# Performance work log

Measured on AMD Instinct MI355X. Metric: run time of the kernel, lower is better.

The kernel has to match this reference:

```python
import jax, jax.numpy as jnp
import numpy as np

N_NODES = 50000
N_EDGES = 800000
IN_FEATS = 256
OUT_FEATS = 32
NUM_HEADS = 8
NUM_ETYPES = 5


def setup_inputs() -> dict:
    key = jax.random.key(0)
    k1, k2, k3, k4, k5, k6 = jax.random.split(key, 6)
    feat = jax.random.normal(k1, (N_NODES, IN_FEATS), dtype=jnp.float32)
    # xavier_normal-ish scale for fc weight [H*D, in]
    fc_w = jax.random.normal(k2, (NUM_HEADS * OUT_FEATS, IN_FEATS), dtype=jnp.float32) * 0.088
    edge_emb = jax.random.normal(k3, (NUM_ETYPES, NUM_HEADS), dtype=jnp.float32)
    e_feat = jax.random.randint(k4, (N_EDGES,), 0, NUM_ETYPES)
    src = jax.random.randint(k5, (N_EDGES,), 0, N_NODES)
    dst = jax.random.randint(k6, (N_EDGES,), 0, N_NODES)
    return {"feat": feat, "fc_w": fc_w, "edge_emb": edge_emb,
            "e_feat": e_feat, "src": src, "dst": dst}


def reference(feat, fc_w, edge_emb, e_feat, src, dst):
    N = feat.shape[0]
    H, D = NUM_HEADS, OUT_FEATS
    # fc: [N, in] @ [in, H*D] -> [N, H, D]
    feat_src = (feat @ fc_w.T).reshape(N, H, D)
    # per-edge, per-head logits from edge-type embedding: [E, H]
    e = edge_emb[e_feat]
    # edge_softmax: softmax over incoming edges of each dst node, per head
    m = jax.ops.segment_max(e, dst, num_segments=N)          # [N, H]
    ex = jnp.exp(e - m[dst])                                  # [E, H]
    denom = jax.ops.segment_sum(ex, dst, num_segments=N)     # [N, H]
    attn = ex / denom[dst]                                    # [E, H]
    # attn_sum: sum of attention weights arriving at each dst (== 1 w/o dropout)
    attn_sum = jax.ops.segment_sum(attn, dst, num_segments=N)  # [N, H]
    # weighted aggregation: sum_e attn_e * feat_src[src_e]
    msg = feat_src[src] * attn[:, :, None]                    # [E, H, D]
    agg = jax.ops.segment_sum(msg, dst, num_segments=N)      # [N, H, D]
    rst = agg / (attn_sum[:, :, None] + 1e-12)
    return rst, attn
```

## Files before the change

kernel.cpp:

```cpp
#include <hip/hip_runtime.h>

typedef unsigned short u16;
typedef unsigned int u32;
typedef __attribute__((ext_vector_type(8))) short bf16x8;
typedef __attribute__((ext_vector_type(4))) float f32x4;
typedef __attribute__((ext_vector_type(2))) float f32x2;

#define NND 50000
#define NE 800000
#define NH 8
#define ND 32
#define NTY 5

__device__ inline u16 f2bf(float x){
  u32 u = __float_as_uint(x);
  return (u16)((u + 0x7FFFu + ((u >> 16) & 1u)) >> 16);
}

__global__ __launch_bounds__(512, 4) void gemm_k(const float* __restrict__ A,
                                                 const float* __restrict__ W,
                                                 u16* __restrict__ C, int M){
  __shared__ float As[128 * 64];
  __shared__ u16  Ws[256 * 64];
  const int tid  = threadIdx.x;
  const int m0   = blockIdx.x * 128;
  const int lane = tid & 63, wid = tid >> 6;
  const int wm = (wid >> 2) * 64, wn = (wid & 3) * 64;
  const int ml = lane & 15, quad = lane >> 4;

  f32x4 acc[4][4] = {};

  const int ra = tid >> 2, ca = (tid & 3) * 4;
  int rag = m0 + ra; if (rag >= M) rag = M - 1;
  const float* aRow = A + (size_t)rag * 256;
  const int rw = tid >> 1, hw = tid & 1;
  const float* wRow = W + (size_t)rw * 256;

  for (int k0 = 0; k0 < 256; k0 += 64){
    #pragma unroll
    for (int q = 0; q < 4; q++){
      float4 v = *(const float4*)(aRow + k0 + (ca + q) * 4);
      *(float4*)(As + ra * 64 + (((ca + q) ^ (ra & 15)) * 4)) = v;
    }
    #pragma unroll
    for (int q = 0; q < 4; q++){
      int ck = hw * 4 + q;
      float4 u0 = *(const float4*)(wRow + k0 + ck * 8);
      float4 u1 = *(const float4*)(wRow + k0 + ck * 8 + 4);
      ushort4 h0 = make_ushort4(f2bf(u0.x), f2bf(u0.y), f2bf(u0.z), f2bf(u0.w));
      ushort4 h1 = make_ushort4(f2bf(u1.x), f2bf(u1.y), f2bf(u1.z), f2bf(u1.w));
      int cp = ck ^ (rw & 7);
      *(ushort4*)(Ws + rw * 64 + cp * 8) = h0;
      *(ushort4*)(Ws + rw * 64 + cp * 8 + 4) = h1;
    }
    __syncthreads();
    #pragma unroll
    for (int kk = 0; kk < 64; kk += 32){
      bf16x8 af[4], wf[4];
      #pragma unroll
      for (int t = 0; t < 4; t++){
        int r = wm + t * 16 + ml;
        int c0 = (kk >> 2) + quad * 2;
        float4 x0 = *(const float4*)(As + r * 64 + (((c0    ) ^ (r & 15)) * 4));
        float4 x1 = *(const float4*)(As + r * 64 + (((c0 + 1) ^ (r & 15)) * 4));
        af[t] = (bf16x8){ (short)f2bf(x0.x), (short)f2bf(x0.y), (short)f2bf(x0.z), (short)f2bf(x0.w),
                          (short)f2bf(x1.x), (short)f2bf(x1.y), (short)f2bf(x1.z), (short)f2bf(x1.w) };
      }
      #pragma unroll
      for (int t = 0; t < 4; t++){
        int n = wn + t * 16 + ml;
        int c = (kk >> 3) + quad;
        wf[t] = *(const bf16x8*)(Ws + n * 64 + ((c ^ (n & 7)) * 8));
      }
      #pragma unroll
      for (int i = 0; i < 4; i++)
        #pragma unroll
        for (int j = 0; j < 4; j++)
          acc[i][j] = __builtin_amdgcn_mfma_f32_16x16x32_bf16(af[i], wf[j], acc[i][j], 0, 0, 0);
    }
    __syncthreads();
  }
  const size_t qoff = (size_t)(wn >> 6) * NND * 64;
  #pragma unroll
  for (int i = 0; i < 4; i++){
    #pragma unroll
    for (int rr = 0; rr < 4; rr++){
      int row = m0 + wm + i * 16 + quad * 4 + rr;
      if (row < M){
        u16* crow = C + qoff + (size_t)row * 64;
        #pragma unroll
        for (int j = 0; j < 4; j++)
          crow[j * 16 + ml] = f2bf(acc[i][j][rr]);
      }
    }
  }
}

__global__ __launch_bounds__(256) void count_k(const int* __restrict__ dst,
                                               int* __restrict__ deg,
                                               int* __restrict__ epos){
  int e = blockIdx.x * 256 + threadIdx.x;
  if (e < NE) epos[e] = atomicAdd(&deg[dst[e]], 1);
}

__global__ __launch_bounds__(256) void scan1_k(const int* __restrict__ deg,
                                               int* __restrict__ offs,
                                               int* __restrict__ bsum){
  __shared__ int lds[256];
  int b = blockIdx.x, tid = threadIdx.x;
  int base = b * 1024 + tid * 4;
  int d[4]; int tsum = 0;
  #pragma unroll
  for (int j = 0; j < 4; j++){
    int node = base + j;
    int v = (node < NND) ? deg[node] : 0;
    d[j] = tsum; tsum += v;
  }
  lds[tid] = tsum; __syncthreads();
  for (int off = 1; off < 256; off <<= 1){
    int v = (tid >= off) ? lds[tid - off] : 0;
    __syncthreads();
    lds[tid] += v;
    __syncthreads();
  }
  int excl = lds[tid] - tsum;
  #pragma unroll
  for (int j = 0; j < 4; j++)
    if (base + j < NND) offs[base + j] = excl + d[j];
  if (tid == 255) bsum[b] = lds[tid];
}

__global__ __launch_bounds__(64) void scan2_k(const int* __restrict__ bsum,
                                              int* __restrict__ bbase, int nb){
  __shared__ int l[64];
  int tid = threadIdx.x;
  int v = (tid < nb) ? bsum[tid] : 0;
  l[tid] = v; __syncthreads();
  for (int off = 1; off < 64; off <<= 1){
    int u = (tid >= off) ? l[tid - off] : 0;
    __syncthreads();
    l[tid] += u;
    __syncthreads();
  }
  bbase[tid] = l[tid] - v;
}

__global__ __launch_bounds__(256) void scatter_k(const int* __restrict__ dst,
                                                 const int* __restrict__ src,
                                                 const int* __restrict__ ef,
                                                 const int* __restrict__ epos,
                                                 const int* __restrict__ offs,
                                                 const int* __restrict__ bbase,
                                                 int* __restrict__ csr){
  int e = blockIdx.x * 256 + threadIdx.x;
  if (e >= NE) return;
  int d = dst[e];
  int pos = offs[d] + bbase[d >> 10] + epos[e];
  csr[pos] = (src[e] << 7) | ef[e];
}

__global__ __launch_bounds__(256) void attn_k(const int* __restrict__ dst,
                                              const int* __restrict__ ef,
                                              const float* __restrict__ rd,
                                              const float* __restrict__ emb,
                                              float* __restrict__ attn){
  __shared__ float wl[40];
  int tid = threadIdx.x;
  if (tid < 40){
    int t = tid >> 3, h = tid & 7;
    float m = emb[h];
    for (int tt = 1; tt < NTY; ++tt) m = fmaxf(m, emb[tt * 8 + h]);
    wl[tid] = expf(emb[t * 8 + h] - m);
  }
  __syncthreads();
  int e = blockIdx.x * 256 + tid;
  if (e >= NE) return;
  int d = dst[e], t = ef[e];
  float4 r0 = *(const float4*)(rd + (size_t)d * 8);
  float4 r1 = *(const float4*)(rd + (size_t)d * 8 + 4);
  const float* wr = wl + t * 8;
  *(float4*)(attn + (size_t)e * 8)     = make_float4(wr[0]*r0.x, wr[1]*r0.y, wr[2]*r0.z, wr[3]*r0.w);
  *(float4*)(attn + (size_t)e * 8 + 4) = make_float4(wr[4]*r1.x, wr[5]*r1.y, wr[6]*r1.z, wr[7]*r1.w);
}

__device__ inline void acc8(uint4 v, float wt, f32x2* a){
  f32x2 w2; w2.x = wt; w2.y = wt;
  f32x2 t0; t0.x = __uint_as_float(v.x << 16); t0.y = __uint_as_float(v.x & 0xFFFF0000u);
  f32x2 t1; t1.x = __uint_as_float(v.y << 16); t1.y = __uint_as_float(v.y & 0xFFFF0000u);
  f32x2 t2; t2.x = __uint_as_float(v.z << 16); t2.y = __uint_as_float(v.z & 0xFFFF0000u);
  f32x2 t3; t3.x = __uint_as_float(v.w << 16); t3.y = __uint_as_float(v.w & 0xFFFF0000u);
  a[0] += w2 * t0; a[1] += w2 * t1; a[2] += w2 * t2; a[3] += w2 * t3;
}

#define NBLK ((NND + 31) / 32)

__global__ __launch_bounds__(256) void agg_k(const u16* __restrict__ fsrc,
                                             const int* __restrict__ csr,
                                             const int* __restrict__ offs,
                                             const int* __restrict__ bbase,
                                             const int* __restrict__ deg,
                                             const float* __restrict__ emb,
                                             float* __restrict__ rst,
                                             float* __restrict__ rd){
  __shared__ float wl[40];
  int tid = threadIdx.x;
  if (tid < 40){
    int t = tid >> 3, h = tid & 7;
    float m = emb[h];
    for (int tt = 1; tt < NTY; ++tt) m = fmaxf(m, emb[tt * 8 + h]);
    wl[tid] = expf(emb[t * 8 + h] - m);
  }
  __syncthreads();
  const int q  = blockIdx.x / NBLK;
  const int nb = blockIdx.x % NBLK;
  int node = nb * 32 + (tid >> 3);
  if (node >= NND) return;
  const int sl = tid & 7;
  const int h  = 2 * q + (sl >> 2);
  const u16* qbase = fsrc + (size_t)q * (NND * 64) + sl * 8;
  int s = offs[node] + bbase[node >> 10];
  int e = s + deg[node];
  f32x2 a[4]; a[0] = 0.f; a[1] = 0.f; a[2] = 0.f; a[3] = 0.f;
  float ss = 0.f;
  int i = s;
  for (; i + 3 < e; i += 4){
    int p0 = csr[i], p1 = csr[i+1], p2 = csr[i+2], p3 = csr[i+3];
    uint4 v0 = *(const uint4*)(qbase + ((size_t)(p0 >> 7) << 6));
    uint4 v1 = *(const uint4*)(qbase + ((size_t)(p1 >> 7) << 6));
    uint4 v2 = *(const uint4*)(qbase + ((size_t)(p2 >> 7) << 6));
    uint4 v3 = *(const uint4*)(qbase + ((size_t)(p3 >> 7) << 6));
    float w0 = wl[(p0 & 7) * 8 + h];
    float w1 = wl[(p1 & 7) * 8 + h];
    float w2 = wl[(p2 & 7) * 8 + h];
    float w3 = wl[(p3 & 7) * 8 + h];
    acc8(v0, w0, a); acc8(v1, w1, a); acc8(v2, w2, a); acc8(v3, w3, a);
    ss += (w0 + w1) + (w2 + w3);
  }
  for (; i < e; i++){
    int p0 = csr[i];
    uint4 v0 = *(const uint4*)(qbase + ((size_t)(p0 >> 7) << 6));
    float w0 = wl[(p0 & 7) * 8 + h];
    acc8(v0, w0, a);
    ss += w0;
  }
  float inv = 1.0f / (ss + 1e-12f);
  float* orow = rst + (size_t)node * 256 + q * 64 + sl * 8;
  *(float4*)(orow)     = make_float4(a[0].x*inv, a[0].y*inv, a[1].x*inv, a[1].y*inv);
  *(float4*)(orow + 4) = make_float4(a[2].x*inv, a[2].y*inv, a[3].x*inv, a[3].y*inv);
  if ((sl & 3) == 0) rd[(size_t)node * 8 + h] = inv;
}

extern "C" void kernel_launch(void* const* d_in, const int* in_sizes, int n_in,
                              void* d_out, int out_size, void* d_ws, size_t ws_size,
                              hipStream_t stream) {
  const float* feat = (const float*)d_in[0];
  const float* fcw  = (const float*)d_in[1];
  const float* emb  = (const float*)d_in[2];
  const int*   ef   = (const int*)d_in[3];
  const int*   src  = (const int*)d_in[4];
  const int*   dst  = (const int*)d_in[5];

  float* rst  = (float*)d_out;
  float* attn = (float*)d_out + (size_t)NND * NH * ND;

  char* ws = (char*)d_ws;
  size_t o = 0;
  u16* fsrc    = (u16*)(ws + o);   o += (size_t)NND * 256 * 2;
  int* csr     = (int*)(ws + o);   o += (size_t)NE * 4;
  int* epos    = (int*)(ws + o);   o += (size_t)NE * 4;
  int* offs    = (int*)(ws + o);   o += 200064;
  int* deg     = (int*)(ws + o);   o += 200064;
  float* rd    = (float*)(ws + o); o += (size_t)NND * NH * 4;
  int* bsum    = (int*)(ws + o);   o += 256;
  int* bbase   = (int*)(ws + o);   o += 256;

  hipMemsetAsync(deg, 0, (size_t)NND * 4, stream);

  gemm_k<<<391, 512, 0, stream>>>(feat, fcw, fsrc, NND);
  count_k<<<(NE + 255) / 256, 256, 0, stream>>>(dst, deg, epos);
  scan1_k<<<(NND + 1023) / 1024, 256, 0, stream>>>(deg, offs, bsum);
  scan2_k<<<1, 64, 0, stream>>>(bsum, bbase, (NND + 1023) / 1024);
  scatter_k<<<(NE + 255) / 256, 256, 0, stream>>>(dst, src, ef, epos, offs, bbase, csr);
  agg_k<<<4 * NBLK, 256, 0, stream>>>(fsrc, csr, offs, bbase, deg, emb, rst, rd);
  attn_k<<<(NE + 255) / 256, 256, 0, stream>>>(dst, ef, rd, emb, attn);
}
```

Baseline: 276.7 us.

## Pre-convert weights to bf16, stage A as bf16 in LDS, add nontemporal I/O

```diff
diff --git a/kernel.cpp b/kernel.cpp
--- a/kernel.cpp
+++ b/kernel.cpp
@@ -17,11 +17,19 @@
   return (u16)((u + 0x7FFFu + ((u >> 16) & 1u)) >> 16);
 }
 
+__global__ __launch_bounds__(256) void wcvt_k(const float* __restrict__ W,
+                                              u16* __restrict__ Wb){
+  int i = (blockIdx.x * 256 + threadIdx.x) * 4;
+  f32x4 v = __builtin_nontemporal_load((const f32x4*)(W + i));
+  ushort4 h = make_ushort4(f2bf(v[0]), f2bf(v[1]), f2bf(v[2]), f2bf(v[3]));
+  *(ushort4*)(Wb + i) = h;
+}
+
 __global__ __launch_bounds__(512, 4) void gemm_k(const float* __restrict__ A,
-                                                 const float* __restrict__ W,
+                                                 const u16* __restrict__ Wb,
                                                  u16* __restrict__ C, int M){
-  __shared__ float As[128 * 64];
-  __shared__ u16  Ws[256 * 64];
+  __shared__ u16 As[128 * 64];
+  __shared__ u16 Ws[256 * 64];
   const int tid  = threadIdx.x;
   const int m0   = blockIdx.x * 128;
   const int lane = tid & 63, wid = tid >> 6;
@@ -30,47 +38,44 @@
 
   f32x4 acc[4][4] = {};
 
-  const int ra = tid >> 2, ca = (tid & 3) * 4;
+  const int ra = tid >> 2, ca0 = (tid & 3) * 2;
   int rag = m0 + ra; if (rag >= M) rag = M - 1;
   const float* aRow = A + (size_t)rag * 256;
   const int rw = tid >> 1, hw = tid & 1;
-  const float* wRow = W + (size_t)rw * 256;
+  const u16* wRow = Wb + (size_t)rw * 256;
 
   for (int k0 = 0; k0 < 256; k0 += 64){
     #pragma unroll
-    for (int q = 0; q < 4; q++){
-      float4 v = *(const float4*)(aRow + k0 + (ca + q) * 4);
-      *(float4*)(As + ra * 64 + (((ca + q) ^ (ra & 15)) * 4)) = v;
+    for (int q = 0; q < 2; q++){
+      int ch = ca0 + q;
+      f32x4 v0 = __builtin_nontemporal_load((const f32x4*)(aRow + k0 + ch * 8));
+      f32x4 v1 = __builtin_nontemporal_load((const f32x4*)(aRow + k0 + ch * 8 + 4));
+      ushort4 h0 = make_ushort4(f2bf(v0[0]), f2bf(v0[1]), f2bf(v0[2]), f2bf(v0[3]));
+      ushort4 h1 = make_ushort4(f2bf(v1[0]), f2bf(v1[1]), f2bf(v1[2]), f2bf(v1[3]));
+      u16* p = As + ra * 64 + ((ch ^ (ra & 7)) * 8);
+      *(ushort4*)p = h0;
+      *(ushort4*)(p + 4) = h1;
     }
     #pragma unroll
     for (int q = 0; q < 4; q++){
-      int ck = hw * 4 + q;
-      float4 u0 = *(const float4*)(wRow + k0 + ck * 8);
-      float4 u1 = *(const float4*)(wRow + k0 + ck * 8 + 4);
-      ushort4 h0 = make_ushort4(f2bf(u0.x), f2bf(u0.y), f2bf(u0.z), f2bf(u0.w));
-      ushort4 h1 = make_ushort4(f2bf(u1.x), f2bf(u1.y), f2bf(u1.z), f2bf(u1.w));
-      int cp = ck ^ (rw & 7);
-      *(ushort4*)(Ws + rw * 64 + cp * 8) = h0;
-      *(ushort4*)(Ws + rw * 64 + cp * 8 + 4) = h1;
+      int ch = hw * 4 + q;
+      uint4 wv = *(const uint4*)(wRow + k0 + ch * 8);
+      *(uint4*)(Ws + rw * 64 + ((ch ^ (rw & 7)) * 8)) = wv;
     }
     __syncthreads();
     #pragma unroll
     for (int kk = 0; kk < 64; kk += 32){
       bf16x8 af[4], wf[4];
+      const int cA = (kk >> 3) + quad;
       #pragma unroll
       for (int t = 0; t < 4; t++){
         int r = wm + t * 16 + ml;
-        int c0 = (kk >> 2) + quad * 2;
-        float4 x0 = *(const float4*)(As + r * 64 + (((c0    ) ^ (r & 15)) * 4));
-        float4 x1 = *(const float4*)(As + r * 64 + (((c0 + 1) ^ (r & 15)) * 4));
-        af[t] = (bf16x8){ (short)f2bf(x0.x), (short)f2bf(x0.y), (short)f2bf(x0.z), (short)f2bf(x0.w),
-                          (short)f2bf(x1.x), (short)f2bf(x1.y), (short)f2bf(x1.z), (short)f2bf(x1.w) };
+        af[t] = *(const bf16x8*)(As + r * 64 + ((cA ^ (r & 7)) * 8));
       }
       #pragma unroll
       for (int t = 0; t < 4; t++){
         int n = wn + t * 16 + ml;
-        int c = (kk >> 3) + quad;
-        wf[t] = *(const bf16x8*)(Ws + n * 64 + ((c ^ (n & 7)) * 8));
+        wf[t] = *(const bf16x8*)(Ws + n * 64 + ((cA ^ (n & 7)) * 8));
       }
       #pragma unroll
       for (int i = 0; i < 4; i++)
@@ -90,7 +95,7 @@
         u16* crow = C + qoff + (size_t)row * 64;
         #pragma unroll
         for (int j = 0; j < 4; j++)
-          crow[j * 16 + ml] = f2bf(acc[i][j][rr]);
+          __builtin_nontemporal_store(f2bf(acc[i][j][rr]), crow + j * 16 + ml);
       }
     }
   }
@@ -161,7 +166,7 @@
 
 __global__ __launch_bounds__(256) void attn_k(const int* __restrict__ dst,
                                               const int* __restrict__ ef,
-                                              const float* __restrict__ rd,
+                                              const float* __restrict__ rdq,
                                               const float* __restrict__ emb,
                                               float* __restrict__ attn){
   __shared__ float wl[40];
@@ -176,11 +181,17 @@
   int e = blockIdx.x * 256 + tid;
   if (e >= NE) return;
   int d = dst[e], t = ef[e];
-  float4 r0 = *(const float4*)(rd + (size_t)d * 8);
-  float4 r1 = *(const float4*)(rd + (size_t)d * 8 + 4);
   const float* wr = wl + t * 8;
-  *(float4*)(attn + (size_t)e * 8)     = make_float4(wr[0]*r0.x, wr[1]*r0.y, wr[2]*r0.z, wr[3]*r0.w);
-  *(float4*)(attn + (size_t)e * 8 + 4) = make_float4(wr[4]*r1.x, wr[5]*r1.y, wr[6]*r1.z, wr[7]*r1.w);
+  f32x4 o0, o1;
+  #pragma unroll
+  for (int q = 0; q < 4; q++){
+    float2 rv = *(const float2*)(rdq + ((size_t)q * NND + d) * 2);
+    float a = wr[2 * q] * rv.x, b = wr[2 * q + 1] * rv.y;
+    if (q < 2){ o0[2 * q] = a; o0[2 * q + 1] = b; }
+    else      { o1[2 * (q - 2)] = a; o1[2 * (q - 2) + 1] = b; }
+  }
+  __builtin_nontemporal_store(o0, (f32x4*)(attn + (size_t)e * 8));
+  __builtin_nontemporal_store(o1, (f32x4*)(attn + (size_t)e * 8 + 4));
 }
 
 __device__ inline void acc8(uint4 v, float wt, f32x2* a){
@@ -193,6 +204,7 @@
 }
 
 #define NBLK ((NND + 31) / 32)
+#define NBLKP (((NBLK + 7) / 8) * 8)
 
 __global__ __launch_bounds__(256) void agg_k(const u16* __restrict__ fsrc,
                                              const int* __restrict__ csr,
@@ -201,7 +213,7 @@
                                              const int* __restrict__ deg,
                                              const float* __restrict__ emb,
                                              float* __restrict__ rst,
-                                             float* __restrict__ rd){
+                                             float* __restrict__ rdq){
   __shared__ float wl[40];
   int tid = threadIdx.x;
   if (tid < 40){
@@ -211,8 +223,9 @@
     wl[tid] = expf(emb[t * 8 + h] - m);
   }
   __syncthreads();
-  const int q  = blockIdx.x / NBLK;
-  const int nb = blockIdx.x % NBLK;
+  const int q  = blockIdx.x / NBLKP;
+  const int nb = blockIdx.x % NBLKP;
+  if (nb >= NBLK) return;
   int node = nb * 32 + (tid >> 3);
   if (node >= NND) return;
   const int sl = tid & 7;
@@ -244,10 +257,14 @@
     ss += w0;
   }
   float inv = 1.0f / (ss + 1e-12f);
+  f32x4 o0, o1;
+  o0[0] = a[0].x*inv; o0[1] = a[0].y*inv; o0[2] = a[1].x*inv; o0[3] = a[1].y*inv;
+  o1[0] = a[2].x*inv; o1[1] = a[2].y*inv; o1[2] = a[3].x*inv; o1[3] = a[3].y*inv;
   float* orow = rst + (size_t)node * 256 + q * 64 + sl * 8;
-  *(float4*)(orow)     = make_float4(a[0].x*inv, a[0].y*inv, a[1].x*inv, a[1].y*inv);
-  *(float4*)(orow + 4) = make_float4(a[2].x*inv, a[2].y*inv, a[3].x*inv, a[3].y*inv);
-  if ((sl & 3) == 0) rd[(size_t)node * 8 + h] = inv;
+  __builtin_nontemporal_store(o0, (f32x4*)orow);
+  __builtin_nontemporal_store(o1, (f32x4*)(orow + 4));
+  if ((sl & 3) == 0)
+    __builtin_nontemporal_store(inv, rdq + ((size_t)q * NND + node) * 2 + (sl >> 2));
 }
 
 extern "C" void kernel_launch(void* const* d_in, const int* in_sizes, int n_in,
@@ -270,17 +287,19 @@
   int* epos    = (int*)(ws + o);   o += (size_t)NE * 4;
   int* offs    = (int*)(ws + o);   o += 200064;
   int* deg     = (int*)(ws + o);   o += 200064;
-  float* rd    = (float*)(ws + o); o += (size_t)NND * NH * 4;
+  float* rdq   = (float*)(ws + o); o += (size_t)NND * NH * 4;
+  u16* wb      = (u16*)(ws + o);   o += (size_t)256 * 256 * 2;
   int* bsum    = (int*)(ws + o);   o += 256;
   int* bbase   = (int*)(ws + o);   o += 256;
 
   hipMemsetAsync(deg, 0, (size_t)NND * 4, stream);
 
-  gemm_k<<<391, 512, 0, stream>>>(feat, fcw, fsrc, NND);
+  wcvt_k<<<64, 256, 0, stream>>>(fcw, wb);
+  gemm_k<<<391, 512, 0, stream>>>(feat, wb, fsrc, NND);
   count_k<<<(NE + 255) / 256, 256, 0, stream>>>(dst, deg, epos);
   scan1_k<<<(NND + 1023) / 1024, 256, 0, stream>>>(deg, offs, bsum);
   scan2_k<<<1, 64, 0, stream>>>(bsum, bbase, (NND + 1023) / 1024);
   scatter_k<<<(NE + 255) / 256, 256, 0, stream>>>(dst, src, ef, epos, offs, bbase, csr);
-  agg_k<<<4 * NBLK, 256, 0, stream>>>(fsrc, csr, offs, bbase, deg, emb, rst, rd);
-  attn_k<<<(NE + 255) / 256, 256, 0, stream>>>(dst, ef, rd, emb, attn);
-}
+  agg_k<<<4 * NBLKP, 256, 0, stream>>>(fsrc, csr, offs, bbase, deg, emb, rst, rdq);
+  attn_k<<<(NE + 255) / 256, 256, 0, stream>>>(dst, ef, rdq, emb, attn);
+}
```

Measured after the change: 270.8 us. -2.1%, faster.
